# Performance work log

Hardware: AMD Instinct MI355X
Metric: run time of the kernel (lower is better)

Reference implementation:

```python
import jax, jax.numpy as jnp
import numpy as np

B, S, D_IN, D = 4, 4096, 768, 64

def setup_inputs() -> dict:
    key = jax.random.key(0)
    kx, kq, kk, kv = jax.random.split(key, 4)
    std = 0.02
    return {
        "x": jax.random.normal(kx, (B, S, D_IN), dtype=jnp.float32),
        "wq": jax.random.normal(kq, (D_IN, D), dtype=jnp.float32) * std,
        "wk": jax.random.normal(kk, (D_IN, D), dtype=jnp.float32) * std,
        "wv": jax.random.normal(kv, (D_IN, D), dtype=jnp.float32) * std,
    }

def reference(x, wq, wk, wv):
    # q,k,v: [B,S,d]
    q = jnp.einsum('bsi,id->bsd', x, wq)
    k = jnp.einsum('bsi,id->bsd', x, wk)
    v = jnp.einsum('bsi,id->bsd', x, wv)
    scale = 1.0 / np.sqrt(q.shape[-1]).astype(np.float32)
    scores = jnp.einsum('bqd,bkd->bqk', q, k) * scale  # [B,S,S]
    attn = jax.nn.softmax(scores, axis=-1)
    return jnp.einsum('bqk,bkd->bqd', attn, v)  # [B,S,d]
```

## Files before the change

kernel.cpp:

```cpp
#include <hip/hip_runtime.h>
#include <hip/hip_bf16.h>

#define B_   4
#define S_   4096
#define DIN  768
#define DH   64

typedef float f32x4 __attribute__((ext_vector_type(4)));
typedef short s16x8 __attribute__((ext_vector_type(8)));
typedef unsigned short u16;

__device__ __forceinline__ u16 f2bf(float f) {
  union { float f; unsigned int u; } a; a.f = f;
  unsigned int u = a.u;
  unsigned int r = (u + 0x7fffu + ((u >> 16) & 1u)) >> 16;
  return (u16)r;
}

__device__ __forceinline__ unsigned int bfpack2(float a, float b) {
  union { float f; unsigned int u; } ua, ub; ua.f = a; ub.f = b;
  return ((ua.u + 0x8000u) >> 16) | ((ub.u + 0x8000u) & 0xffff0000u);
}

__device__ __forceinline__ s16x8 ld8s(const u16* p) {
  return *reinterpret_cast<const s16x8*>(p);
}

__device__ __forceinline__ s16x8 pack8(float4 a, float4 b) {
  s16x8 h;
  h[0] = (short)f2bf(a.x); h[1] = (short)f2bf(a.y);
  h[2] = (short)f2bf(a.z); h[3] = (short)f2bf(a.w);
  h[4] = (short)f2bf(b.x); h[5] = (short)f2bf(b.y);
  h[6] = (short)f2bf(b.z); h[7] = (short)f2bf(b.w);
  return h;
}

#define GLD_LDS(gp, lp) \
  __builtin_amdgcn_global_load_lds((const __attribute__((address_space(1))) void*)(gp), \
                                   (__attribute__((address_space(3))) void*)(lp), 16, 0, 0)

__global__ void prep_w(const float* __restrict__ wq, const float* __restrict__ wk,
                       const float* __restrict__ wv, u16* __restrict__ wt) {
  int tid = blockIdx.x * 256 + threadIdx.x;
  if (tid >= 192 * DIN) return;
  int n = tid / DIN, k = tid % DIN;
  const float* src; float scale = 1.0f; int col;
  if (n < 64)       { src = wq; col = n;       scale = 0.125f; }
  else if (n < 128) { src = wk; col = n - 64;  }
  else              { src = wv; col = n - 128; }
  float v = src[k * DH + col] * scale;
  int chunk = k & ~63;
  int kin = k & 63;
  int gr = (kin >> 3) ^ (n & 7);
  wt[n * DIN + chunk + gr * 8 + (kin & 7)] = f2bf(v);
}

__global__ __launch_bounds__(256) void qkv_gemm(const float* __restrict__ x,
    const u16* __restrict__ wt, u16* __restrict__ qb, u16* __restrict__ kb,
    u16* __restrict__ vt) {
  __shared__ __align__(16) u16 xl[2][32 * 72];
  __shared__ __align__(16) u16 wl[2][192 * 64];
  int t = threadIdx.x;
  int w = t >> 6, l = t & 63, g = l >> 4, lq = l & 15;
  int wr = w >> 1, wc = w & 1;
  int m0 = blockIdx.x * 32;
  int xrow = t >> 3, xc = t & 7;

  f32x4 acc[6];
#pragma unroll
  for (int i = 0; i < 6; i++) acc[i] = f32x4{0.f, 0.f, 0.f, 0.f};

  const float* xp0 = x + (size_t)(m0 + xrow) * DIN + xc * 8;

  {
    float4 xa = *reinterpret_cast<const float4*>(xp0);
    float4 xb = *reinterpret_cast<const float4*>(xp0 + 4);
#pragma unroll
    for (int i = 0; i < 6; i++) {
      int tau = i * 4 + w; int n = 8 * tau + (l >> 3);
      GLD_LDS(wt + n * DIN + (l & 7) * 8, &wl[0][tau * 512]);
    }
    *reinterpret_cast<s16x8*>(&xl[0][xrow * 72 + xc * 8]) = pack8(xa, xb);
    asm volatile("s_waitcnt vmcnt(0)" ::: "memory");
    __syncthreads();
  }

  for (int ks = 0; ks < 12; ks++) {
    int cur = ks & 1;
    bool more = ks < 11;
    float4 na, nb;
    if (more) {
      int k1 = (ks + 1) * 64;
      na = *reinterpret_cast<const float4*>(xp0 + k1);
      nb = *reinterpret_cast<const float4*>(xp0 + k1 + 4);
#pragma unroll
      for (int i = 0; i < 6; i++) {
        int tau = i * 4 + w; int n = 8 * tau + (l >> 3);
        GLD_LDS(wt + n * DIN + k1 + (l & 7) * 8, &wl[cur ^ 1][tau * 512]);
      }
    }
    s16x8 a0 = ld8s(&xl[cur][(16 * wr + lq) * 72 + g * 8]);
    s16x8 a1 = ld8s(&xl[cur][(16 * wr + lq) * 72 + g * 8 + 32]);
#pragma unroll
    for (int nt = 0; nt < 6; nt++) {
      int n = wc * 96 + nt * 16 + lq;
      s16x8 b0 = ld8s(&wl[cur][n * 64 + ((g ^ (n & 7)) * 8)]);
      s16x8 b1 = ld8s(&wl[cur][n * 64 + (((g + 4) ^ (n & 7)) * 8)]);
      acc[nt] = __builtin_amdgcn_mfma_f32_16x16x32_bf16(a0, b0, acc[nt], 0, 0, 0);
      acc[nt] = __builtin_amdgcn_mfma_f32_16x16x32_bf16(a1, b1, acc[nt], 0, 0, 0);
    }
    if (more) {
      asm volatile("s_waitcnt vmcnt(0)" ::: "memory");
      *reinterpret_cast<s16x8*>(&xl[cur ^ 1][xrow * 72 + xc * 8]) = pack8(na, nb);
      __syncthreads();
    }
  }

  int b = m0 >> 12;
  int srow0 = (m0 & (S_ - 1)) + 16 * wr + 4 * g;
#pragma unroll
  for (int nt = 0; nt < 6; nt++) {
    int col = wc * 96 + nt * 16 + lq;
    u16* base; int c;
    if (col < 64)       { base = qb; c = col; }
    else if (col < 128) { base = kb; c = col - 64; }
    else                { base = vt; c = col - 128; }
#pragma unroll
    for (int r = 0; r < 4; r++) {
      int srow = srow0 + r;
      u16 hv = f2bf(acc[nt][r]);
      if (col < 128) {
        int gr = (c >> 3) ^ (srow & 7);
        base[(size_t)(b * S_ + srow) * DH + gr * 8 + (c & 7)] = hv;
      } else {
        int gr = ((srow >> 3) & 7) ^ (c & 7);
        base[(size_t)(b * DH + c) * S_ + (srow & ~63) + gr * 8 + (srow & 7)] = hv;
      }
    }
  }
}

__global__ __launch_bounds__(512) void attn(const u16* __restrict__ qb,
    const u16* __restrict__ kb, const u16* __restrict__ vt, float* __restrict__ out) {
  __shared__ __align__(16) u16 smem[41984];

  int t = threadIdx.x;
  int w8 = t >> 6, half = w8 >> 2, w = w8 & 3, l = t & 63, g = l >> 4, lq = l & 15;
  int bq = blockIdx.x;
  int b = bq >> 6;
  int q0 = (bq & 63) * 64;
  int kvbase = half * 2048;

  int sq = q0 + 16 * w + lq;
  const u16* qrow = qb + (size_t)(b * S_ + sq) * DH;
  s16x8 qa0 = ld8s(qrow + ((g ^ (sq & 7)) * 8));
  s16x8 qa1 = ld8s(qrow + (((g + 4) ^ (sq & 7)) * 8));

  u16* pl = smem + 32768 + w8 * 1152;

  float mrun = -1e30f, lrun = 0.f;
  f32x4 acco[4];
#pragma unroll
  for (int nt = 0; nt < 4; nt++) acco[nt] = f32x4{0.f, 0.f, 0.f, 0.f};

  int tau0 = w * 2;
  int srow_st = 8 * tau0 + (l >> 3);
  int gcol = (l & 7) * 8;

  {
    u16* dst = smem + half * 16384;
#pragma unroll
    for (int i = 0; i < 2; i++) {
      int row = srow_st + 8 * i;
      GLD_LDS(kb + (size_t)(b * S_ + kvbase + row) * DH + gcol, &dst[(tau0 + i) * 512]);
      GLD_LDS(vt + (size_t)(b * DH + row) * S_ + kvbase + gcol, &dst[4096 + (tau0 + i) * 512]);
    }
    asm volatile("s_waitcnt vmcnt(0)" ::: "memory");
    __syncthreads();
  }

  const float L2E = 1.44269504f;

  for (int it = 0; it < 32; it++) {
    int cur = it & 1;
    bool more = it < 31;
    if (more) {
      int k1 = kvbase + (it + 1) * 64;
      u16* dst = smem + half * 16384 + (cur ^ 1) * 8192;
#pragma unroll
      for (int i = 0; i < 2; i++) {
        int row = srow_st + 8 * i;
        GLD_LDS(kb + (size_t)(b * S_ + k1 + row) * DH + gcol, &dst[(tau0 + i) * 512]);
        GLD_LDS(vt + (size_t)(b * DH + row) * S_ + k1 + gcol, &dst[4096 + (tau0 + i) * 512]);
      }
    }
    const u16* kl = smem + half * 16384 + cur * 8192;
    const u16* vl = kl + 4096;

    f32x4 accs[4];
#pragma unroll
    for (int kt = 0; kt < 4; kt++) {
      int krow = kt * 16 + lq;
      s16x8 kf0 = ld8s(&kl[krow * 64 + ((g ^ (krow & 7)) * 8)]);
      s16x8 kf1 = ld8s(&kl[krow * 64 + (((g + 4) ^ (krow & 7)) * 8)]);
      f32x4 c = f32x4{0.f, 0.f, 0.f, 0.f};
      c = __builtin_amdgcn_mfma_f32_16x16x32_bf16(kf0, qa0, c, 0, 0, 0);
      c = __builtin_amdgcn_mfma_f32_16x16x32_bf16(kf1, qa1, c, 0, 0, 0);
      accs[kt] = c;
    }

    float mx = fmaxf(fmaxf(accs[0][0], accs[0][1]), fmaxf(accs[0][2], accs[0][3]));
#pragma unroll
    for (int kt = 1; kt < 4; kt++)
      mx = fmaxf(mx, fmaxf(fmaxf(accs[kt][0], accs[kt][1]),
                           fmaxf(accs[kt][2], accs[kt][3])));
    mx = fmaxf(mx, __shfl_xor(mx, 16));
    mx = fmaxf(mx, __shfl_xor(mx, 32));
    float mnew = fmaxf(mrun, mx);
    float scale = exp2f((mrun - mnew) * L2E);
    float sc0 = __shfl(scale, 4 * g + 0);
    float sc1 = __shfl(scale, 4 * g + 1);
    float sc2 = __shfl(scale, 4 * g + 2);
    float sc3 = __shfl(scale, 4 * g + 3);

    float s = 0.f;
#pragma unroll
    for (int kt = 0; kt < 4; kt++) {
#pragma unroll
      for (int r = 0; r < 4; r++) {
        float e = exp2f((accs[kt][r] - mnew) * L2E);
        accs[kt][r] = e; s += e;
      }
    }
    s += __shfl_xor(s, 16);
    s += __shfl_xor(s, 32);
    lrun = lrun * scale + s;
    mrun = mnew;

#pragma unroll
    for (int kt = 0; kt < 4; kt++) {
      uint2 u;
      u.x = bfpack2(accs[kt][0], accs[kt][1]);
      u.y = bfpack2(accs[kt][2], accs[kt][3]);
      *reinterpret_cast<uint2*>(&pl[lq * 72 + kt * 16 + 4 * g]) = u;
    }
    asm volatile("s_waitcnt lgkmcnt(0)" ::: "memory");

#pragma unroll
    for (int nt = 0; nt < 4; nt++) {
      acco[nt][0] *= sc0; acco[nt][1] *= sc1;
      acco[nt][2] *= sc2; acco[nt][3] *= sc3;
    }

    s16x8 pa0 = ld8s(&pl[lq * 72 + g * 8]);
    s16x8 pa1 = ld8s(&pl[lq * 72 + 32 + g * 8]);
#pragma unroll
    for (int nt = 0; nt < 4; nt++) {
      int d = nt * 16 + lq;
      s16x8 vf0 = ld8s(&vl[d * 64 + ((g ^ (d & 7)) * 8)]);
      s16x8 vf1 = ld8s(&vl[d * 64 + (((g + 4) ^ (d & 7)) * 8)]);
      acco[nt] = __builtin_amdgcn_mfma_f32_16x16x32_bf16(pa0, vf0, acco[nt], 0, 0, 0);
      acco[nt] = __builtin_amdgcn_mfma_f32_16x16x32_bf16(pa1, vf1, acco[nt], 0, 0, 0);
    }
    if (more) {
      asm volatile("s_waitcnt vmcnt(0)" ::: "memory");
      __syncthreads();
    }
  }

  __syncthreads();
  float* mO = reinterpret_cast<float*>(smem);
  float* mM = reinterpret_cast<float*>(smem) + 4096;
  float* mL = mM + 64;

  if (half == 1) {
#pragma unroll
    for (int nt = 0; nt < 4; nt++)
#pragma unroll
      for (int r = 0; r < 4; r++)
        mO[(16 * w + 4 * g + r) * 64 + nt * 16 + lq] = acco[nt][r];
    if (g == 0) {
      mM[16 * w + lq] = mrun;
      mL[16 * w + lq] = lrun;
    }
  }
  __syncthreads();
  if (half == 0) {
#pragma unroll
    for (int r = 0; r < 4; r++) {
      int row = 16 * w + 4 * g + r;
      float m1 = __shfl(mrun, 4 * g + r);
      float l1 = __shfl(lrun, 4 * g + r);
      float m2 = mM[row], l2 = mL[row];
      float m = fmaxf(m1, m2);
      float f1 = exp2f((m1 - m) * 1.44269504f);
      float f2 = exp2f((m2 - m) * 1.44269504f);
      float inv = 1.0f / (l1 * f1 + l2 * f2);
#pragma unroll
      for (int nt = 0; nt < 4; nt++) {
        float val = (acco[nt][r] * f1 + mO[row * 64 + nt * 16 + lq] * f2) * inv;
        out[(size_t)(b * S_ + q0 + row) * DH + nt * 16 + lq] = val;
      }
    }
  }
}

extern "C" void kernel_launch(void* const* d_in, const int* in_sizes, int n_in,
                              void* d_out, int out_size, void* d_ws, size_t ws_size,
                              hipStream_t stream) {
  const float* x  = (const float*)d_in[0];
  const float* wq = (const float*)d_in[1];
  const float* wk = (const float*)d_in[2];
  const float* wv = (const float*)d_in[3];
  float* out = (float*)d_out;
  char* ws = (char*)d_ws;

  u16* wt = (u16*)(ws);
  u16* qb = (u16*)(ws + 294912);
  u16* kb = (u16*)(ws + 294912 + 2097152);
  u16* vt = (u16*)(ws + 294912 + 2 * 2097152);

  hipLaunchKernelGGL(prep_w,   dim3(576), dim3(256), 0, stream, wq, wk, wv, wt);
  hipLaunchKernelGGL(qkv_gemm, dim3(512), dim3(256), 0, stream, x, wt, qb, kb, vt);
  hipLaunchKernelGGL(attn,     dim3(256), dim3(512), 0, stream, qb, kb, vt, out);
}
```

Measured before the change: 150.2 us.

## Register-resident x fragments, bpermute P relayout, tiled weight transpose, occupancy hints

Several changes land together. The QKV GEMM now loads each wave's x rows straight into registers as bf16 MFMA fragments, which removes the x LDS staging and its per-step pack/store. The attention kernel reshapes P into A-operand layout with ds_bpermute cross-lane shuffles instead of an LDS write/read round trip, which shrinks shared memory and adds launch_bounds occupancy hints. The weight prep kernel uses an LDS-tiled transpose over 36 blocks. In exchange, register pressure rises (24 s16x8 fragments in the GEMM), and the bpermute path adds many shuffle instructions.

```diff
diff --git a/kernel.cpp b/kernel.cpp
--- a/kernel.cpp
+++ b/kernel.cpp
@@ -8,6 +8,7 @@
 
 typedef float f32x4 __attribute__((ext_vector_type(4)));
 typedef short s16x8 __attribute__((ext_vector_type(8)));
+typedef int   i32x4 __attribute__((ext_vector_type(4)));
 typedef unsigned short u16;
 
 __device__ __forceinline__ u16 f2bf(float f) {
@@ -26,92 +27,97 @@
   return *reinterpret_cast<const s16x8*>(p);
 }
 
-__device__ __forceinline__ s16x8 pack8(float4 a, float4 b) {
-  s16x8 h;
-  h[0] = (short)f2bf(a.x); h[1] = (short)f2bf(a.y);
-  h[2] = (short)f2bf(a.z); h[3] = (short)f2bf(a.w);
-  h[4] = (short)f2bf(b.x); h[5] = (short)f2bf(b.y);
-  h[6] = (short)f2bf(b.z); h[7] = (short)f2bf(b.w);
-  return h;
+__device__ __forceinline__ s16x8 pack8f(float4 a, float4 b) {
+  union { i32x4 i; s16x8 s; } u;
+  u.i[0] = (int)bfpack2(a.x, a.y);
+  u.i[1] = (int)bfpack2(a.z, a.w);
+  u.i[2] = (int)bfpack2(b.x, b.y);
+  u.i[3] = (int)bfpack2(b.z, b.w);
+  return u.s;
 }
 
 #define GLD_LDS(gp, lp) \
   __builtin_amdgcn_global_load_lds((const __attribute__((address_space(1))) void*)(gp), \
                                    (__attribute__((address_space(3))) void*)(lp), 16, 0, 0)
 
-__global__ void prep_w(const float* __restrict__ wq, const float* __restrict__ wk,
-                       const float* __restrict__ wv, u16* __restrict__ wt) {
-  int tid = blockIdx.x * 256 + threadIdx.x;
-  if (tid >= 192 * DIN) return;
-  int n = tid / DIN, k = tid % DIN;
-  const float* src; float scale = 1.0f; int col;
-  if (n < 64)       { src = wq; col = n;       scale = 0.125f; }
-  else if (n < 128) { src = wk; col = n - 64;  }
-  else              { src = wv; col = n - 128; }
-  float v = src[k * DH + col] * scale;
-  int chunk = k & ~63;
-  int kin = k & 63;
-  int gr = (kin >> 3) ^ (n & 7);
-  wt[n * DIN + chunk + gr * 8 + (kin & 7)] = f2bf(v);
-}
-
-__global__ __launch_bounds__(256) void qkv_gemm(const float* __restrict__ x,
+__global__ __launch_bounds__(256) void prep_w(const float* __restrict__ wq,
+    const float* __restrict__ wk, const float* __restrict__ wv, u16* __restrict__ wt) {
+  __shared__ u16 tl[64 * 65];
+  int bid = blockIdx.x;
+  int mtx = bid / 12;
+  int k0 = (bid % 12) * 64;
+  const float* src = (mtx == 0) ? wq : (mtx == 1) ? wk : wv;
+  float scale = (mtx == 0) ? 0.125f : 1.0f;
+  int t = threadIdx.x;
+  int rr = t >> 6, cc = t & 63;
+#pragma unroll
+  for (int i = 0; i < 16; i++) {
+    int kr = i * 4 + rr;
+    tl[kr * 65 + cc] = f2bf(src[(size_t)(k0 + kr) * 64 + cc] * scale);
+  }
+  __syncthreads();
+  int nbase = mtx * 64;
+#pragma unroll
+  for (int i = 0; i < 16; i++) {
+    int nl = i * 4 + rr;
+    int n = nbase + nl;
+    int gr = (cc >> 3) ^ (n & 7);
+    wt[(size_t)n * DIN + k0 + gr * 8 + (cc & 7)] = tl[cc * 65 + nl];
+  }
+}
+
+__global__ __launch_bounds__(256, 3) void qkv_gemm(const float* __restrict__ x,
     const u16* __restrict__ wt, u16* __restrict__ qb, u16* __restrict__ kb,
     u16* __restrict__ vt) {
-  __shared__ __align__(16) u16 xl[2][32 * 72];
   __shared__ __align__(16) u16 wl[2][192 * 64];
   int t = threadIdx.x;
   int w = t >> 6, l = t & 63, g = l >> 4, lq = l & 15;
   int wr = w >> 1, wc = w & 1;
   int m0 = blockIdx.x * 32;
-  int xrow = t >> 3, xc = t & 7;
+
+#pragma unroll
+  for (int i = 0; i < 6; i++) {
+    int tau = i * 4 + w; int n = 8 * tau + (l >> 3);
+    GLD_LDS(wt + n * DIN + (l & 7) * 8, &wl[0][tau * 512]);
+  }
+
+  const float* xrowp = x + (size_t)(m0 + 16 * wr + lq) * DIN + g * 8;
+  s16x8 af[24];
+#pragma unroll
+  for (int c = 0; c < 24; c++) {
+    float4 a = *reinterpret_cast<const float4*>(xrowp + c * 32);
+    float4 b = *reinterpret_cast<const float4*>(xrowp + c * 32 + 4);
+    af[c] = pack8f(a, b);
+  }
 
   f32x4 acc[6];
 #pragma unroll
   for (int i = 0; i < 6; i++) acc[i] = f32x4{0.f, 0.f, 0.f, 0.f};
 
-  const float* xp0 = x + (size_t)(m0 + xrow) * DIN + xc * 8;
-
-  {
-    float4 xa = *reinterpret_cast<const float4*>(xp0);
-    float4 xb = *reinterpret_cast<const float4*>(xp0 + 4);
-#pragma unroll
-    for (int i = 0; i < 6; i++) {
-      int tau = i * 4 + w; int n = 8 * tau + (l >> 3);
-      GLD_LDS(wt + n * DIN + (l & 7) * 8, &wl[0][tau * 512]);
-    }
-    *reinterpret_cast<s16x8*>(&xl[0][xrow * 72 + xc * 8]) = pack8(xa, xb);
-    asm volatile("s_waitcnt vmcnt(0)" ::: "memory");
-    __syncthreads();
-  }
-
+  asm volatile("s_waitcnt vmcnt(0)" ::: "memory");
+  __syncthreads();
+
+#pragma unroll
   for (int ks = 0; ks < 12; ks++) {
     int cur = ks & 1;
-    bool more = ks < 11;
-    float4 na, nb;
-    if (more) {
+    if (ks < 11) {
       int k1 = (ks + 1) * 64;
-      na = *reinterpret_cast<const float4*>(xp0 + k1);
-      nb = *reinterpret_cast<const float4*>(xp0 + k1 + 4);
 #pragma unroll
       for (int i = 0; i < 6; i++) {
         int tau = i * 4 + w; int n = 8 * tau + (l >> 3);
         GLD_LDS(wt + n * DIN + k1 + (l & 7) * 8, &wl[cur ^ 1][tau * 512]);
       }
     }
-    s16x8 a0 = ld8s(&xl[cur][(16 * wr + lq) * 72 + g * 8]);
-    s16x8 a1 = ld8s(&xl[cur][(16 * wr + lq) * 72 + g * 8 + 32]);
 #pragma unroll
     for (int nt = 0; nt < 6; nt++) {
       int n = wc * 96 + nt * 16 + lq;
       s16x8 b0 = ld8s(&wl[cur][n * 64 + ((g ^ (n & 7)) * 8)]);
       s16x8 b1 = ld8s(&wl[cur][n * 64 + (((g + 4) ^ (n & 7)) * 8)]);
-      acc[nt] = __builtin_amdgcn_mfma_f32_16x16x32_bf16(a0, b0, acc[nt], 0, 0, 0);
-      acc[nt] = __builtin_amdgcn_mfma_f32_16x16x32_bf16(a1, b1, acc[nt], 0, 0, 0);
-    }
-    if (more) {
+      acc[nt] = __builtin_amdgcn_mfma_f32_16x16x32_bf16(af[2 * ks], b0, acc[nt], 0, 0, 0);
+      acc[nt] = __builtin_amdgcn_mfma_f32_16x16x32_bf16(af[2 * ks + 1], b1, acc[nt], 0, 0, 0);
+    }
+    if (ks < 11) {
       asm volatile("s_waitcnt vmcnt(0)" ::: "memory");
-      *reinterpret_cast<s16x8*>(&xl[cur ^ 1][xrow * 72 + xc * 8]) = pack8(na, nb);
       __syncthreads();
     }
   }
@@ -140,9 +146,9 @@
   }
 }
 
-__global__ __launch_bounds__(512) void attn(const u16* __restrict__ qb,
+__global__ __launch_bounds__(512, 4) void attn(const u16* __restrict__ qb,
     const u16* __restrict__ kb, const u16* __restrict__ vt, float* __restrict__ out) {
-  __shared__ __align__(16) u16 smem[41984];
+  __shared__ __align__(16) u16 smem[32768];
 
   int t = threadIdx.x;
   int w8 = t >> 6, half = w8 >> 2, w = w8 & 3, l = t & 63, g = l >> 4, lq = l & 15;
@@ -156,7 +162,10 @@
   s16x8 qa0 = ld8s(qrow + ((g ^ (sq & 7)) * 8));
   s16x8 qa1 = ld8s(qrow + (((g + 4) ^ (sq & 7)) * 8));
 
-  u16* pl = smem + 32768 + w8 * 1152;
+  int sA = ((2 * (g & 1)) << 4) | lq;
+  int idxA = sA << 2;
+  int idxB = idxA + 64;
+  bool chi = ((g >> 1) & 1);
 
   float mrun = -1e30f, lrun = 0.f;
   f32x4 acco[4];
@@ -209,11 +218,13 @@
       accs[kt] = c;
     }
 
-    float mx = fmaxf(fmaxf(accs[0][0], accs[0][1]), fmaxf(accs[0][2], accs[0][3]));
-#pragma unroll
-    for (int kt = 1; kt < 4; kt++)
-      mx = fmaxf(mx, fmaxf(fmaxf(accs[kt][0], accs[kt][1]),
-                           fmaxf(accs[kt][2], accs[kt][3])));
+    f32x4 m4 = accs[0];
+#pragma unroll
+    for (int kt = 1; kt < 4; kt++) {
+      m4[0] = fmaxf(m4[0], accs[kt][0]); m4[1] = fmaxf(m4[1], accs[kt][1]);
+      m4[2] = fmaxf(m4[2], accs[kt][2]); m4[3] = fmaxf(m4[3], accs[kt][3]);
+    }
+    float mx = fmaxf(fmaxf(m4[0], m4[1]), fmaxf(m4[2], m4[3]));
     mx = fmaxf(mx, __shfl_xor(mx, 16));
     mx = fmaxf(mx, __shfl_xor(mx, 32));
     float mnew = fmaxf(mrun, mx);
@@ -237,14 +248,37 @@
     lrun = lrun * scale + s;
     mrun = mnew;
 
-#pragma unroll
-    for (int kt = 0; kt < 4; kt++) {
-      uint2 u;
-      u.x = bfpack2(accs[kt][0], accs[kt][1]);
-      u.y = bfpack2(accs[kt][2], accs[kt][3]);
-      *reinterpret_cast<uint2*>(&pl[lq * 72 + kt * 16 + 4 * g]) = u;
-    }
-    asm volatile("s_waitcnt lgkmcnt(0)" ::: "memory");
+    int pk0 = (int)bfpack2(accs[0][0], accs[0][1]);
+    int pk1 = (int)bfpack2(accs[0][2], accs[0][3]);
+    int pk2 = (int)bfpack2(accs[1][0], accs[1][1]);
+    int pk3 = (int)bfpack2(accs[1][2], accs[1][3]);
+    int pk4 = (int)bfpack2(accs[2][0], accs[2][1]);
+    int pk5 = (int)bfpack2(accs[2][2], accs[2][3]);
+    int pk6 = (int)bfpack2(accs[3][0], accs[3][1]);
+    int pk7 = (int)bfpack2(accs[3][2], accs[3][3]);
+
+    int fA0 = __builtin_amdgcn_ds_bpermute(idxA, pk0);
+    int fA1 = __builtin_amdgcn_ds_bpermute(idxA, pk1);
+    int fA2 = __builtin_amdgcn_ds_bpermute(idxA, pk2);
+    int fA3 = __builtin_amdgcn_ds_bpermute(idxA, pk3);
+    int fA4 = __builtin_amdgcn_ds_bpermute(idxA, pk4);
+    int fA5 = __builtin_amdgcn_ds_bpermute(idxA, pk5);
+    int fA6 = __builtin_amdgcn_ds_bpermute(idxA, pk6);
+    int fA7 = __builtin_amdgcn_ds_bpermute(idxA, pk7);
+    int fB0 = __builtin_amdgcn_ds_bpermute(idxB, pk0);
+    int fB1 = __builtin_amdgcn_ds_bpermute(idxB, pk1);
+    int fB2 = __builtin_amdgcn_ds_bpermute(idxB, pk2);
+    int fB3 = __builtin_amdgcn_ds_bpermute(idxB, pk3);
+    int fB4 = __builtin_amdgcn_ds_bpermute(idxB, pk4);
+    int fB5 = __builtin_amdgcn_ds_bpermute(idxB, pk5);
+    int fB6 = __builtin_amdgcn_ds_bpermute(idxB, pk6);
+    int fB7 = __builtin_amdgcn_ds_bpermute(idxB, pk7);
+
+    union { i32x4 i; s16x8 h; } upa0, upa1;
+    upa0.i[0] = chi ? fA2 : fA0;  upa0.i[1] = chi ? fA3 : fA1;
+    upa0.i[2] = chi ? fB2 : fB0;  upa0.i[3] = chi ? fB3 : fB1;
+    upa1.i[0] = chi ? fA6 : fA4;  upa1.i[1] = chi ? fA7 : fA5;
+    upa1.i[2] = chi ? fB6 : fB4;  upa1.i[3] = chi ? fB7 : fB5;
 
 #pragma unroll
     for (int nt = 0; nt < 4; nt++) {
@@ -252,15 +286,13 @@
       acco[nt][2] *= sc2; acco[nt][3] *= sc3;
     }
 
-    s16x8 pa0 = ld8s(&pl[lq * 72 + g * 8]);
-    s16x8 pa1 = ld8s(&pl[lq * 72 + 32 + g * 8]);
 #pragma unroll
     for (int nt = 0; nt < 4; nt++) {
       int d = nt * 16 + lq;
       s16x8 vf0 = ld8s(&vl[d * 64 + ((g ^ (d & 7)) * 8)]);
       s16x8 vf1 = ld8s(&vl[d * 64 + (((g + 4) ^ (d & 7)) * 8)]);
-      acco[nt] = __builtin_amdgcn_mfma_f32_16x16x32_bf16(pa0, vf0, acco[nt], 0, 0, 0);
-      acco[nt] = __builtin_amdgcn_mfma_f32_16x16x32_bf16(pa1, vf1, acco[nt], 0, 0, 0);
+      acco[nt] = __builtin_amdgcn_mfma_f32_16x16x32_bf16(upa0.h, vf0, acco[nt], 0, 0, 0);
+      acco[nt] = __builtin_amdgcn_mfma_f32_16x16x32_bf16(upa1.h, vf1, acco[nt], 0, 0, 0);
     }
     if (more) {
       asm volatile("s_waitcnt vmcnt(0)" ::: "memory");
@@ -320,7 +352,7 @@
   u16* kb = (u16*)(ws + 294912 + 2097152);
   u16* vt = (u16*)(ws + 294912 + 2 * 2097152);
 
-  hipLaunchKernelGGL(prep_w,   dim3(576), dim3(256), 0, stream, wq, wk, wv, wt);
+  hipLaunchKernelGGL(prep_w,   dim3(36),  dim3(256), 0, stream, wq, wk, wv, wt);
   hipLaunchKernelGGL(qkv_gemm, dim3(512), dim3(256), 0, stream, x, wt, qb, kb, vt);
   hipLaunchKernelGGL(attn,     dim3(256), dim3(512), 0, stream, qb, kb, vt, out);
 }
```

New measurement: 159.1 us. +5.9%, slower.
